# Kernel optimization log

Measured on AMD Instinct MI355X. Metric: run time of the kernel, lower is better.

Reference implementation:

```python
import jax, jax.numpy as jnp
import numpy as np

NUM_TAGS = 19
START_ID = 17  # lbl_to_id['START_LBL']
PAD_ID = 18    # lbl_to_id['PAD_LBL']
NEG = -1000.0


def setup_inputs() -> dict:
    key = jax.random.key(0)
    k1, k2, k3 = jax.random.split(key, 3)
    B, L = 512, 2048
    P = jax.random.normal(k1, (B, L, NUM_TAGS), dtype=jnp.float32)
    T = jax.random.normal(k2, (NUM_TAGS, NUM_TAGS), dtype=jnp.float32)
    # contiguous-prefix valid mask, lengths in [1, L]
    lengths = jax.random.randint(k3, (B,), 1, L + 1)
    mask = jnp.arange(L)[None, :] < lengths[:, None]  # [B, L] bool
    return {"P": P, "T": T, "mask": mask}


def _viterbi_forward(P, T, mask):
    # P: [B, L, K] emissions; T[j, k] = score of transition prev=k -> cur=j
    B, L, K = P.shape
    DP0 = jnp.full((B, K), NEG, dtype=P.dtype).at[:, START_ID].set(0.0)

    def step(DP, xs):
        emit, m = xs  # emit: [B, K], m: [B] bool
        scores = DP[:, None, :] + T[None, :, :]        # [B, cur, prev]
        best = scores.max(axis=-1)                      # [B, K]
        arg = scores.argmax(axis=-1).astype(jnp.int32)  # [B, K] backpointers
        new_DP = best + emit
        DP = jnp.where(m[:, None], new_DP, DP)          # frozen past sequence end
        return DP, arg

    DP, choice = jax.lax.scan(
        step, DP0, (jnp.swapaxes(P, 0, 1), jnp.swapaxes(mask, 0, 1))
    )  # choice: [L, B, K]
    DP = DP + T[PAD_ID][None, :]  # transition into PAD at the end
    return DP, choice


def reference(P, T, mask):
    B, L, K = P.shape
    DP, choice = _viterbi_forward(P, T, mask)
    last = DP.argmax(axis=-1).astype(jnp.int32)          # [B] best final tag
    lengths = mask.sum(axis=-1).astype(jnp.int32)        # [B]
    bidx = jnp.arange(B)

    def back(c, t):
        # path[t] = choice[t+1][path[t+1]] for t < len-1; path[len-1] = last
        nxt = choice[jnp.minimum(t + 1, L - 1), bidx, c]  # [B]
        new_c = jnp.where(t < lengths - 1, nxt, c)
        out = jnp.where(t < lengths, new_c, -1)           # -1 pads beyond length
        return new_c, out

    _, outs = jax.lax.scan(back, last, jnp.arange(L - 1, -1, -1))  # [L, B]
    path = jnp.flip(jnp.swapaxes(outs, 0, 1), axis=1)  # [B, L], decoded tags
    return path
```

## Files before the change

kernel.cpp:

```cpp
#include <hip/hip_runtime.h>

#define Bn 512
#define Ln 2048
#define Kn 19
#define NEGV (-1000.0f)
#define START_IDn 17
#define PAD_IDn 18
#define SEG 64
#define PBYTES 79691776u


#define DP_CORE(BASE)                                                          \
    float4 q0 = *(const float4*)((BASE) + 0);                                  \
    float4 q1 = *(const float4*)((BASE) + 4);                                  \
    float4 q2 = *(const float4*)((BASE) + 8);                                  \
    float4 q3 = *(const float4*)((BASE) + 12);                                 \
    float4 q4 = *(const float4*)((BASE) + 16);            \
    float cand[Kn];                                                            \
    cand[0]  = q0.x + Trow[0];  cand[1]  = q0.y + Trow[1];                     \
    cand[2]  = q0.z + Trow[2];  cand[3]  = q0.w + Trow[3];                     \
    cand[4]  = q1.x + Trow[4];  cand[5]  = q1.y + Trow[5];                     \
    cand[6]  = q1.z + Trow[6];  cand[7]  = q1.w + Trow[7];                     \
    cand[8]  = q2.x + Trow[8];  cand[9]  = q2.y + Trow[9];                     \
    cand[10] = q2.z + Trow[10]; cand[11] = q2.w + Trow[11];                    \
    cand[12] = q3.x + Trow[12]; cand[13] = q3.y + Trow[13];                    \
    cand[14] = q3.z + Trow[14]; cand[15] = q3.w + Trow[15];                    \
    cand[16] = q4.x + Trow[16]; cand[17] = q4.y + Trow[17];                    \
    cand[18] = q4.z + Trow[18];                                                \
    float m0 = fmaxf(fmaxf(cand[0],  cand[1]),  cand[2]);                      \
    float m1 = fmaxf(fmaxf(cand[3],  cand[4]),  cand[5]);                      \
    float m2 = fmaxf(fmaxf(cand[6],  cand[7]),  cand[8]);                      \
    float m3 = fmaxf(fmaxf(cand[9],  cand[10]), cand[11]);                     \
    float m4 = fmaxf(fmaxf(cand[12], cand[13]), cand[14]);                     \
    float m5 = fmaxf(fmaxf(cand[15], cand[16]), cand[17]);                     \
    float n0 = fmaxf(fmaxf(m0, m1), m2);                                       \
    float n1 = fmaxf(fmaxf(m3, m4), cand[18]);                                 \
    float best = fmaxf(fmaxf(n0, n1), m5);

__global__ __launch_bounds__(64, 1) void crf_fwd(
    const float* __restrict__ P, const float* __restrict__ T,
    const int* __restrict__ mask, float* __restrict__ dpck,
    float* __restrict__ dpfin, int* __restrict__ lens)
{
    const int lane = threadIdx.x;
    const int half = lane >> 5;
    const int c = lane & 31;
    const int b = blockIdx.x * 2 + half;
    const int cc = (c < Kn) ? c : (Kn - 1);

    float Trow[Kn];
#pragma unroll
    for (int p = 0; p < Kn; ++p) Trow[p] = T[cc * Kn + p];

    const int* mrow = mask + (size_t)b * Ln;
    int sum = 0;
#pragma unroll
    for (int j = 0; j < Ln / 128; ++j) {
        int4 v = *(const int4*)(mrow + j * 128 + c * 4);
        sum += v.x + v.y + v.z + v.w;
    }
#pragma unroll
    for (int k = 1; k < 32; k <<= 1) sum += __shfl_xor(sum, k, 64);
    const int len = sum;
    if (c == 0) lens[b] = len;
    const int lenO = __shfl_xor(len, 32, 64);
    int maxlen = len > lenO ? len : lenO;
    int lmin = len < lenO ? len : lenO;
    lmin = __builtin_amdgcn_readfirstlane(lmin);
    int mlen = (maxlen + (SEG - 1)) & ~(SEG - 1);
    mlen = __builtin_amdgcn_readfirstlane(mlen);

    __shared__ float dp[2][32];
    __shared__ float ebuf[2][2][1280];

    float mydp = (c == START_IDn) ? 0.0f : NEGV;
    dp[half][c] = mydp;

    const unsigned bbyte = (unsigned)b * (Ln * Kn * 4u);
    const unsigned limit = PBYTES - 16;
    const char* Pc = (const char*)P;
    float4 r[10];

#define STAGE_LOAD(ci)                                                         \
    { unsigned base_ = bbyte + (unsigned)(ci) * 4864u + ((unsigned)c << 4);    \
      _Pragma("unroll")                                                        \
      for (int i_ = 0; i_ < 10; ++i_) {                                        \
          unsigned o_ = base_ + (unsigned)i_ * 512u;                           \
          if (o_ > limit) o_ = limit;                                          \
          r[i_] = *(const float4*)(Pc + o_);                                   \
      } }
#define STAGE_WRITE(nb)                                                        \
    { float* d_ = &ebuf[nb][half][(unsigned)c << 2];                           \
      _Pragma("unroll")                                                        \
      for (int i_ = 0; i_ < 10; ++i_) *(float4*)(d_ + i_ * 128) = r[i_]; }

    int buf = 0;
    STAGE_LOAD(0);
    STAGE_WRITE(0);

    for (int t0 = 0; t0 < mlen; t0 += SEG) {
        if (c < Kn)
            dpck[((unsigned)b * 32u + (unsigned)(t0 >> 6)) * (unsigned)Kn + (unsigned)c] = mydp;
        STAGE_LOAD((t0 >> 6) + 1);
        const float* ebl = &ebuf[buf][half][0];

        if (t0 + SEG <= lmin) {
            for (int tt = 0; tt < SEG; tt += 8) {
#pragma unroll
                for (int u = 0; u < 8; ++u) {
                    const float e = ebl[(tt + u) * Kn + cc];
                    const float* base_ = &dp[half][0];
                    DP_CORE(base_)
                    mydp = best + e;
                    dp[half][c] = mydp;
                }
            }
        } else {
            for (int tt = 0; tt < SEG; tt += 8) {
#pragma unroll
                for (int u = 0; u < 8; ++u) {
                    const int t = t0 + tt + u;
                    const float e = ebl[(tt + u) * Kn + cc];
                    const float* base_ = &dp[half][0];
                    DP_CORE(base_)
                    float nd = best + e;
                    mydp = (t < len) ? nd : mydp;
                    dp[half][c] = mydp;
                }
            }
        }
        STAGE_WRITE(buf ^ 1);
        buf ^= 1;
    }
    if (c < Kn) dpfin[b * Kn + c] = mydp;
#undef STAGE_LOAD
#undef STAGE_WRITE
}

__global__ __launch_bounds__(256) void crf_rec(
    const float* __restrict__ P, const float* __restrict__ T,
    const float* __restrict__ dpck, const int* __restrict__ lens,
    unsigned char* __restrict__ choice)
{
    const int tid = threadIdx.x;
    const int halfid = tid >> 5;
    const int c = tid & 31;
    const int cc = (c < Kn) ? c : (Kn - 1);
    const int task = blockIdx.x * 8 + halfid;
    const int b = task >> 5;
    const int seg = task & 31;
    const int t0 = seg * SEG;
    const int len = lens[b];
    if (t0 >= len) return;

    __shared__ float dp[8][32];
    __shared__ __align__(16) unsigned char cbuf[8][SEG * Kn];

    float Trow[Kn];
#pragma unroll
    for (int p = 0; p < Kn; ++p) Trow[p] = T[cc * Kn + p];

    float mydp = (c < Kn) ? dpck[((unsigned)b * 32u + (unsigned)seg) * (unsigned)Kn + (unsigned)c]
                          : NEGV;
    dp[halfid][c] = mydp;

    const float* prow = P + (size_t)b * Ln * Kn + (size_t)t0 * Kn;

    float eb[8];
#pragma unroll
    for (int u = 0; u < 8; ++u) eb[u] = prow[u * Kn + cc];

    for (int tt = 0; tt < SEG; tt += 8) {
#pragma unroll
        for (int u = 0; u < 8; ++u) {
            const int t = t0 + tt + u;
            const float e = eb[u];
            const float* base_ = &dp[halfid][0];
            DP_CORE(base_)
            float nd = best + e;
            mydp = (t < len) ? nd : mydp;
            dp[halfid][c] = mydp;

            int arg = Kn - 1;
#pragma unroll
            for (int p = Kn - 2; p >= 0; --p)
                arg = (cand[p] == best) ? p : arg;
            if (c < Kn) cbuf[halfid][(tt + u) * Kn + c] = (unsigned char)arg;

            int tn = tt + u + 8;
            int tloc = (t0 + tn < Ln) ? tn : (Ln - 1 - t0);
            eb[u] = prow[tloc * Kn + cc];
        }
    }
    {
        const int4* s = (const int4*)&cbuf[halfid][0];
        int4* d = (int4*)(choice + (size_t)b * Ln * Kn + (size_t)t0 * Kn);
        for (int i = c; i < (SEG * Kn) / 16; i += 32) d[i] = s[i];
    }
}

__global__ __launch_bounds__(384, 1) void crf_bwd(
    const float* __restrict__ T, const unsigned char* __restrict__ choice,
    const float* __restrict__ dpfin, const int* __restrict__ lens,
    int* __restrict__ out)
{
    __shared__ unsigned char comp[Ln * Kn];
    __shared__ int vchain[17];
    __shared__ int s_last, s_len;

    const int b = blockIdx.x;
    const int tid = threadIdx.x;

    {
        const int4* src = (const int4*)(choice + (size_t)b * Ln * Kn);
        int4* dst = (int4*)comp;
        for (int i = tid; i < (Ln * Kn) / 16; i += 384) dst[i] = src[i];
    }
    if (tid == 0) {
        s_len = lens[b];
        float bestv = dpfin[b * Kn + 0] + T[PAD_IDn * Kn + 0];
        int bl = 0;
        for (int ci = 1; ci < Kn; ++ci) {
            float v = dpfin[b * Kn + ci] + T[PAD_IDn * Kn + ci];
            if (v > bestv) { bestv = v; bl = ci; }
        }
        s_last = bl;
    }
    __syncthreads();
    const int len = s_len;

    {
        const int wv = tid >> 6;
        const int lane = tid & 63;
        const int ch = wv * 3 + lane / Kn;
        const int c = lane % Kn;
        if (lane < 3 * Kn && ch < 16) {
            int cur = c;
            const int tb = ch * 128 + 127;
            for (int i = 0; i < 128; ++i) {
                const int t = tb - i;
                int nv = comp[t * Kn + cur];
                cur = (t < len) ? nv : cur;
                comp[t * Kn + c] = cur;
            }
        }
    }
    __syncthreads();

    if (tid == 0) {
        int v = s_last;
        vchain[16] = v;
        for (int ch = 15; ch >= 0; --ch) {
            v = comp[ch * 128 * Kn + v];
            vchain[ch] = v;
        }
    }
    __syncthreads();

    const int last = s_last;
    int* orow = out + (size_t)b * Ln;
    for (int t = tid; t < Ln; t += 384) {
        int val;
        if (t >= len) {
            val = -1;
        } else if (t == Ln - 1) {
            val = last;
        } else {
            const int tp = t + 1;
            const int vc = vchain[(tp >> 7) + 1];
            val = comp[tp * Kn + vc];
        }
        orow[t] = val;
    }
}

extern "C" void kernel_launch(void* const* d_in, const int* in_sizes, int n_in,
                              void* d_out, int out_size, void* d_ws, size_t ws_size,
                              hipStream_t stream)
{
    const float* P    = (const float*)d_in[0];
    const float* T    = (const float*)d_in[1];
    const int*   mask = (const int*)d_in[2];
    int* out = (int*)d_out;

    const size_t choice_bytes = (size_t)Bn * Ln * Kn;
    unsigned char* choice = (unsigned char*)d_ws;
    float* dpfin = (float*)((char*)d_ws + choice_bytes);
    int* lens = (int*)((char*)d_ws + choice_bytes + (size_t)Bn * Kn * 4);

    float* dpck = (float*)((char*)d_out + 2 * 1024 * 1024);

    crf_fwd<<<Bn / 2, 64, 0, stream>>>(P, T, mask, dpck, dpfin, lens);
    crf_rec<<<(Bn * 32) / 8, 256, 0, stream>>>(P, T, dpck, lens, choice);
    crf_bwd<<<Bn, 384, 0, stream>>>(T, choice, dpfin, lens, out);
}
```

Measured before the change: 398.2 us.

## Use one wave per sequence with readlane broadcast in forward Viterbi

The forward pass now gives each 64-lane wave a single sequence instead of packing two sequences per wave. The 19 previous DP values are broadcast with scalar readlane instead of an LDS store and reload each step. The loop runs only to the sequence's own length, with an exact remainder tail, so the masked select and the wasted steps caused by the longer partner sequence disappear. In exchange the launch uses twice as many blocks, and the 19 readlanes per step may serialise on the scalar path.

```diff
diff --git a/kernel.cpp b/kernel.cpp
--- a/kernel.cpp
+++ b/kernel.cpp
@@ -9,6 +9,118 @@
 #define SEG 64
 #define PBYTES 79691776u
 
+
+__global__ __launch_bounds__(64, 1) void crf_fwd(
+    const float* __restrict__ P, const float* __restrict__ T,
+    const int* __restrict__ mask, float* __restrict__ dpck,
+    float* __restrict__ dpfin, int* __restrict__ lens)
+{
+    const int lane = threadIdx.x;
+    const int b = blockIdx.x;
+    const int cc = (lane < Kn) ? lane : (Kn - 1);
+
+    float Trow[Kn];
+#pragma unroll
+    for (int p = 0; p < Kn; ++p) Trow[p] = T[cc * Kn + p];
+
+    const int* mrow = mask + (size_t)b * Ln;
+    int sum = 0;
+#pragma unroll
+    for (int j = 0; j < 8; ++j) {
+        int4 v = *(const int4*)(mrow + j * 256 + lane * 4);
+        sum += v.x + v.y + v.z + v.w;
+    }
+#pragma unroll
+    for (int k = 1; k < 64; k <<= 1) sum += __shfl_xor(sum, k, 64);
+    int lenr = __builtin_amdgcn_readfirstlane(sum);
+    if (lenr < 1) lenr = 1;
+    if (lenr > Ln) lenr = Ln;
+    const int len = lenr;
+    if (lane == 0) lens[b] = len;
+
+    __shared__ float ebuf[2][1232];
+
+    float mydp = (lane == START_IDn) ? 0.0f : NEGV;
+
+    const unsigned bbyte = (unsigned)b * (Ln * Kn * 4u);
+    const unsigned limit = PBYTES - 16;
+    const char* Pc = (const char*)P;
+    float4 r[5];
+
+#define STAGE_LOAD(ci)                                                         \
+    { unsigned sb_ = bbyte + (unsigned)(ci) * 4864u;                           \
+      _Pragma("unroll")                                                        \
+      for (int i_ = 0; i_ < 5; ++i_) {                                         \
+          unsigned idx_ = (unsigned)lane + 64u * (unsigned)i_;                 \
+          if (idx_ > 303u) idx_ = 303u;                                        \
+          unsigned o_ = sb_ + idx_ * 16u;                                      \
+          if (o_ > limit) o_ = limit;                                          \
+          r[i_] = *(const float4*)(Pc + o_);                                   \
+      } }
+#define STAGE_WRITE(nb)                                                        \
+    { _Pragma("unroll")                                                        \
+      for (int i_ = 0; i_ < 5; ++i_) {                                         \
+          unsigned idx_ = (unsigned)lane + 64u * (unsigned)i_;                 \
+          if (idx_ > 303u) idx_ = 303u;                                        \
+          *(float4*)((char*)&ebuf[nb][0] + idx_ * 16u) = r[i_];                \
+      } }
+
+#define RL(p) __int_as_float(__builtin_amdgcn_readlane(mi_, (p)))
+#define STEP_BODY(EXPR_E)                                                      \
+    { const float e_ = (EXPR_E);                                               \
+      const int mi_ = __float_as_int(mydp);                                    \
+      float c0_  = RL(0)  + Trow[0];  float c1_  = RL(1)  + Trow[1];           \
+      float c2_  = RL(2)  + Trow[2];  float c3_  = RL(3)  + Trow[3];           \
+      float c4_  = RL(4)  + Trow[4];  float c5_  = RL(5)  + Trow[5];           \
+      float c6_  = RL(6)  + Trow[6];  float c7_  = RL(7)  + Trow[7];           \
+      float c8_  = RL(8)  + Trow[8];  float c9_  = RL(9)  + Trow[9];           \
+      float c10_ = RL(10) + Trow[10]; float c11_ = RL(11) + Trow[11];          \
+      float c12_ = RL(12) + Trow[12]; float c13_ = RL(13) + Trow[13];          \
+      float c14_ = RL(14) + Trow[14]; float c15_ = RL(15) + Trow[15];          \
+      float c16_ = RL(16) + Trow[16]; float c17_ = RL(17) + Trow[17];          \
+      float c18_ = RL(18) + Trow[18];                                          \
+      float t0_ = fmaxf(fmaxf(c0_,  c1_),  c2_);                               \
+      float t1_ = fmaxf(fmaxf(c3_,  c4_),  c5_);                               \
+      float t2_ = fmaxf(fmaxf(c6_,  c7_),  c8_);                               \
+      float t3_ = fmaxf(fmaxf(c9_,  c10_), c11_);                              \
+      float t4_ = fmaxf(fmaxf(c12_, c13_), c14_);                              \
+      float t5_ = fmaxf(fmaxf(c15_, c16_), c17_);                              \
+      float u0_ = fmaxf(fmaxf(t0_, t1_), t2_);                                 \
+      float u1_ = fmaxf(fmaxf(t3_, t4_), c18_);                                \
+      float best_ = fmaxf(fmaxf(u0_, u1_), t5_);                               \
+      mydp = best_ + e_; }
+
+    int buf = 0;
+    STAGE_LOAD(0);
+    STAGE_WRITE(0);
+
+    const int nfull = len >> 6;
+    const int rem = len & 63;
+
+    for (int seg = 0; seg < nfull; ++seg) {
+        if (lane < Kn)
+            dpck[((unsigned)b * 32u + (unsigned)seg) * (unsigned)Kn + (unsigned)lane] = mydp;
+        STAGE_LOAD(seg + 1);
+        const float* ebl = &ebuf[buf][0];
+        for (int t8 = 0; t8 < SEG; t8 += 8) {
+#pragma unroll
+            for (int u = 0; u < 8; ++u) STEP_BODY(ebl[(t8 + u) * Kn + cc]);
+        }
+        STAGE_WRITE(buf ^ 1);
+        buf ^= 1;
+    }
+    if (rem) {
+        if (lane < Kn)
+            dpck[((unsigned)b * 32u + (unsigned)nfull) * (unsigned)Kn + (unsigned)lane] = mydp;
+        const float* ebl = &ebuf[buf][0];
+        for (int tt = 0; tt < rem; ++tt) STEP_BODY(ebl[tt * Kn + cc]);
+    }
+    if (lane < Kn) dpfin[b * Kn + lane] = mydp;
+#undef STAGE_LOAD
+#undef STAGE_WRITE
+#undef STEP_BODY
+#undef RL
+}
 
 #define DP_CORE(BASE)                                                          \
     float4 q0 = *(const float4*)((BASE) + 0);                                  \
@@ -37,106 +149,6 @@
     float n1 = fmaxf(fmaxf(m3, m4), cand[18]);                                 \
     float best = fmaxf(fmaxf(n0, n1), m5);
 
-__global__ __launch_bounds__(64, 1) void crf_fwd(
-    const float* __restrict__ P, const float* __restrict__ T,
-    const int* __restrict__ mask, float* __restrict__ dpck,
-    float* __restrict__ dpfin, int* __restrict__ lens)
-{
-    const int lane = threadIdx.x;
-    const int half = lane >> 5;
-    const int c = lane & 31;
-    const int b = blockIdx.x * 2 + half;
-    const int cc = (c < Kn) ? c : (Kn - 1);
-
-    float Trow[Kn];
-#pragma unroll
-    for (int p = 0; p < Kn; ++p) Trow[p] = T[cc * Kn + p];
-
-    const int* mrow = mask + (size_t)b * Ln;
-    int sum = 0;
-#pragma unroll
-    for (int j = 0; j < Ln / 128; ++j) {
-        int4 v = *(const int4*)(mrow + j * 128 + c * 4);
-        sum += v.x + v.y + v.z + v.w;
-    }
-#pragma unroll
-    for (int k = 1; k < 32; k <<= 1) sum += __shfl_xor(sum, k, 64);
-    const int len = sum;
-    if (c == 0) lens[b] = len;
-    const int lenO = __shfl_xor(len, 32, 64);
-    int maxlen = len > lenO ? len : lenO;
-    int lmin = len < lenO ? len : lenO;
-    lmin = __builtin_amdgcn_readfirstlane(lmin);
-    int mlen = (maxlen + (SEG - 1)) & ~(SEG - 1);
-    mlen = __builtin_amdgcn_readfirstlane(mlen);
-
-    __shared__ float dp[2][32];
-    __shared__ float ebuf[2][2][1280];
-
-    float mydp = (c == START_IDn) ? 0.0f : NEGV;
-    dp[half][c] = mydp;
-
-    const unsigned bbyte = (unsigned)b * (Ln * Kn * 4u);
-    const unsigned limit = PBYTES - 16;
-    const char* Pc = (const char*)P;
-    float4 r[10];
-
-#define STAGE_LOAD(ci)                                                         \
-    { unsigned base_ = bbyte + (unsigned)(ci) * 4864u + ((unsigned)c << 4);    \
-      _Pragma("unroll")                                                        \
-      for (int i_ = 0; i_ < 10; ++i_) {                                        \
-          unsigned o_ = base_ + (unsigned)i_ * 512u;                           \
-          if (o_ > limit) o_ = limit;                                          \
-          r[i_] = *(const float4*)(Pc + o_);                                   \
-      } }
-#define STAGE_WRITE(nb)                                                        \
-    { float* d_ = &ebuf[nb][half][(unsigned)c << 2];                           \
-      _Pragma("unroll")                                                        \
-      for (int i_ = 0; i_ < 10; ++i_) *(float4*)(d_ + i_ * 128) = r[i_]; }
-
-    int buf = 0;
-    STAGE_LOAD(0);
-    STAGE_WRITE(0);
-
-    for (int t0 = 0; t0 < mlen; t0 += SEG) {
-        if (c < Kn)
-            dpck[((unsigned)b * 32u + (unsigned)(t0 >> 6)) * (unsigned)Kn + (unsigned)c] = mydp;
-        STAGE_LOAD((t0 >> 6) + 1);
-        const float* ebl = &ebuf[buf][half][0];
-
-        if (t0 + SEG <= lmin) {
-            for (int tt = 0; tt < SEG; tt += 8) {
-#pragma unroll
-                for (int u = 0; u < 8; ++u) {
-                    const float e = ebl[(tt + u) * Kn + cc];
-                    const float* base_ = &dp[half][0];
-                    DP_CORE(base_)
-                    mydp = best + e;
-                    dp[half][c] = mydp;
-                }
-            }
-        } else {
-            for (int tt = 0; tt < SEG; tt += 8) {
-#pragma unroll
-                for (int u = 0; u < 8; ++u) {
-                    const int t = t0 + tt + u;
-                    const float e = ebl[(tt + u) * Kn + cc];
-                    const float* base_ = &dp[half][0];
-                    DP_CORE(base_)
-                    float nd = best + e;
-                    mydp = (t < len) ? nd : mydp;
-                    dp[half][c] = mydp;
-                }
-            }
-        }
-        STAGE_WRITE(buf ^ 1);
-        buf ^= 1;
-    }
-    if (c < Kn) dpfin[b * Kn + c] = mydp;
-#undef STAGE_LOAD
-#undef STAGE_WRITE
-}
-
 __global__ __launch_bounds__(256) void crf_rec(
     const float* __restrict__ P, const float* __restrict__ T,
     const float* __restrict__ dpck, const int* __restrict__ lens,
@@ -290,7 +302,7 @@
 
     float* dpck = (float*)((char*)d_out + 2 * 1024 * 1024);
 
-    crf_fwd<<<Bn / 2, 64, 0, stream>>>(P, T, mask, dpck, dpfin, lens);
+    crf_fwd<<<Bn, 64, 0, stream>>>(P, T, mask, dpck, dpfin, lens);
     crf_rec<<<(Bn * 32) / 8, 256, 0, stream>>>(P, T, dpck, lens, choice);
     crf_bwd<<<Bn, 384, 0, stream>>>(T, choice, dpfin, lens, out);
 }
```

Measured after the change: 475.1 us. +19.3%, slower.

## Stage segment emissions in LDS with bulk float4 loads and trim loop to valid length

Applied to the files above, without the earlier changes.

The recompute kernel now loads each segment's whole emission block (64 steps x 19 tags) into shared memory up front with coalesced float4 loads, replacing the rolling 8-deep register prefetch of scalar global loads. The per-step loop reads emissions from LDS and runs only up to the valid remaining length, which drops the per-step length mask and the work done past the end of each sequence. It adds about 39 KB of LDS per block, which may reduce occupancy, and it places a load barrier at the start of each segment.

```diff
diff --git a/kernel.cpp b/kernel.cpp
--- a/kernel.cpp
+++ b/kernel.cpp
@@ -153,44 +153,56 @@
     const int len = lens[b];
     if (t0 >= len) return;
 
+    int rem = len - t0;
+    if (rem > SEG) rem = SEG;
+
     __shared__ float dp[8][32];
     __shared__ __align__(16) unsigned char cbuf[8][SEG * Kn];
+    __shared__ float ebuf[8][1232];
 
     float Trow[Kn];
 #pragma unroll
     for (int p = 0; p < Kn; ++p) Trow[p] = T[cc * Kn + p];
+
+    {
+        const unsigned sb = ((unsigned)b * (Ln * Kn * 4u)) + (unsigned)t0 * (Kn * 4u);
+        const unsigned limit = PBYTES - 16;
+        const char* Pc = (const char*)P;
+        float4 rr[10];
+#pragma unroll
+        for (int i = 0; i < 10; ++i) {
+            unsigned idx = (unsigned)c + 32u * (unsigned)i;
+            if (idx > 303u) idx = 303u;
+            unsigned o = sb + idx * 16u;
+            if (o > limit) o = limit;
+            rr[i] = *(const float4*)(Pc + o);
+        }
+        char* eb = (char*)&ebuf[halfid][0];
+#pragma unroll
+        for (int i = 0; i < 10; ++i) {
+            unsigned idx = (unsigned)c + 32u * (unsigned)i;
+            if (idx > 303u) idx = 303u;
+            *(float4*)(eb + idx * 16u) = rr[i];
+        }
+    }
 
     float mydp = (c < Kn) ? dpck[((unsigned)b * 32u + (unsigned)seg) * (unsigned)Kn + (unsigned)c]
                           : NEGV;
     dp[halfid][c] = mydp;
 
-    const float* prow = P + (size_t)b * Ln * Kn + (size_t)t0 * Kn;
-
-    float eb[8];
-#pragma unroll
-    for (int u = 0; u < 8; ++u) eb[u] = prow[u * Kn + cc];
-
-    for (int tt = 0; tt < SEG; tt += 8) {
-#pragma unroll
-        for (int u = 0; u < 8; ++u) {
-            const int t = t0 + tt + u;
-            const float e = eb[u];
-            const float* base_ = &dp[halfid][0];
-            DP_CORE(base_)
-            float nd = best + e;
-            mydp = (t < len) ? nd : mydp;
-            dp[halfid][c] = mydp;
-
-            int arg = Kn - 1;
-#pragma unroll
-            for (int p = Kn - 2; p >= 0; --p)
-                arg = (cand[p] == best) ? p : arg;
-            if (c < Kn) cbuf[halfid][(tt + u) * Kn + c] = (unsigned char)arg;
-
-            int tn = tt + u + 8;
-            int tloc = (t0 + tn < Ln) ? tn : (Ln - 1 - t0);
-            eb[u] = prow[tloc * Kn + cc];
-        }
+    const float* ebl = &ebuf[halfid][0];
+    for (int tt = 0; tt < rem; ++tt) {
+        const float e = ebl[tt * Kn + cc];
+        const float* base_ = &dp[halfid][0];
+        DP_CORE(base_)
+        mydp = best + e;
+        dp[halfid][c] = mydp;
+
+        int arg = Kn - 1;
+#pragma unroll
+        for (int p = Kn - 2; p >= 0; --p)
+            arg = (cand[p] == best) ? p : arg;
+        if (c < Kn) cbuf[halfid][tt * Kn + c] = (unsigned char)arg;
     }
     {
         const int4* s = (const int4*)&cbuf[halfid][0];
```

After: 415.5 us. 1.04x slower.

## Fuse segment recompute and backtrace into one kernel keeping backpointers in LDS

Applied to the files above, without the earlier changes.

Merges the per-segment backpointer recomputation kernel with the backtrace kernel. Each block now handles one batch row, and 16 half-waves each recompute two 64-step segments, writing argmax choices straight into a shared-memory buffer instead of global memory. This removes the global write and re-read of the roughly 20 MB choice array and one kernel launch. The cost is lower parallelism: 512 blocks with a two-pass loop, one block per CU because of about 39 KB of LDS, and a serial recompute depth doubled per half-wave. The dpck scratch also moves from the output buffer into the workspace.

```diff
diff --git a/kernel.cpp b/kernel.cpp
--- a/kernel.cpp
+++ b/kernel.cpp
@@ -137,112 +137,90 @@
 #undef STAGE_WRITE
 }
 
-__global__ __launch_bounds__(256) void crf_rec(
+__global__ __launch_bounds__(512, 1) void crf_recbt(
     const float* __restrict__ P, const float* __restrict__ T,
-    const float* __restrict__ dpck, const int* __restrict__ lens,
-    unsigned char* __restrict__ choice)
+    const float* __restrict__ dpck, const float* __restrict__ dpfin,
+    const int* __restrict__ lens, int* __restrict__ out)
 {
     const int tid = threadIdx.x;
-    const int halfid = tid >> 5;
+    const int b = blockIdx.x;
+    const int hw = tid >> 5;
     const int c = tid & 31;
     const int cc = (c < Kn) ? c : (Kn - 1);
-    const int task = blockIdx.x * 8 + halfid;
-    const int b = task >> 5;
-    const int seg = task & 31;
-    const int t0 = seg * SEG;
     const int len = lens[b];
-    if (t0 >= len) return;
-
-    __shared__ float dp[8][32];
-    __shared__ __align__(16) unsigned char cbuf[8][SEG * Kn];
+
+    __shared__ unsigned char comp[Ln * Kn];
+    __shared__ float dp[16][32];
+    __shared__ int vchain[17];
+    __shared__ int s_last;
 
     float Trow[Kn];
 #pragma unroll
     for (int p = 0; p < Kn; ++p) Trow[p] = T[cc * Kn + p];
 
-    float mydp = (c < Kn) ? dpck[((unsigned)b * 32u + (unsigned)seg) * (unsigned)Kn + (unsigned)c]
-                          : NEGV;
-    dp[halfid][c] = mydp;
-
-    const float* prow = P + (size_t)b * Ln * Kn + (size_t)t0 * Kn;
-
-    float eb[8];
-#pragma unroll
-    for (int u = 0; u < 8; ++u) eb[u] = prow[u * Kn + cc];
-
-    for (int tt = 0; tt < SEG; tt += 8) {
-#pragma unroll
-        for (int u = 0; u < 8; ++u) {
-            const int t = t0 + tt + u;
-            const float e = eb[u];
-            const float* base_ = &dp[halfid][0];
-            DP_CORE(base_)
-            float nd = best + e;
-            mydp = (t < len) ? nd : mydp;
-            dp[halfid][c] = mydp;
-
-            int arg = Kn - 1;
-#pragma unroll
-            for (int p = Kn - 2; p >= 0; --p)
-                arg = (cand[p] == best) ? p : arg;
-            if (c < Kn) cbuf[halfid][(tt + u) * Kn + c] = (unsigned char)arg;
-
-            int tn = tt + u + 8;
-            int tloc = (t0 + tn < Ln) ? tn : (Ln - 1 - t0);
-            eb[u] = prow[tloc * Kn + cc];
-        }
-    }
-    {
-        const int4* s = (const int4*)&cbuf[halfid][0];
-        int4* d = (int4*)(choice + (size_t)b * Ln * Kn + (size_t)t0 * Kn);
-        for (int i = c; i < (SEG * Kn) / 16; i += 32) d[i] = s[i];
-    }
-}
-
-__global__ __launch_bounds__(384, 1) void crf_bwd(
-    const float* __restrict__ T, const unsigned char* __restrict__ choice,
-    const float* __restrict__ dpfin, const int* __restrict__ lens,
-    int* __restrict__ out)
-{
-    __shared__ unsigned char comp[Ln * Kn];
-    __shared__ int vchain[17];
-    __shared__ int s_last, s_len;
-
-    const int b = blockIdx.x;
-    const int tid = threadIdx.x;
-
-    {
-        const int4* src = (const int4*)(choice + (size_t)b * Ln * Kn);
-        int4* dst = (int4*)comp;
-        for (int i = tid; i < (Ln * Kn) / 16; i += 384) dst[i] = src[i];
-    }
-    if (tid == 0) {
-        s_len = lens[b];
-        float bestv = dpfin[b * Kn + 0] + T[PAD_IDn * Kn + 0];
-        int bl = 0;
-        for (int ci = 1; ci < Kn; ++ci) {
-            float v = dpfin[b * Kn + ci] + T[PAD_IDn * Kn + ci];
-            if (v > bestv) { bestv = v; bl = ci; }
-        }
-        s_last = bl;
+#pragma unroll 1
+    for (int pass = 0; pass < 2; ++pass) {
+        const int seg = hw + pass * 16;
+        const int t0 = seg * SEG;
+        if (t0 < len) {
+            float mydp = (c < Kn)
+                ? dpck[((unsigned)b * 32u + (unsigned)seg) * (unsigned)Kn + (unsigned)c]
+                : NEGV;
+            dp[hw][c] = mydp;
+            const float* prow = P + (size_t)b * Ln * Kn + (size_t)t0 * Kn;
+
+            float eb[8];
+#pragma unroll
+            for (int u = 0; u < 8; ++u) eb[u] = prow[u * Kn + cc];
+
+            for (int tt = 0; tt < SEG; tt += 8) {
+#pragma unroll
+                for (int u = 0; u < 8; ++u) {
+                    const int t = t0 + tt + u;
+                    const float e = eb[u];
+                    const float* base_ = &dp[hw][0];
+                    DP_CORE(base_)
+                    float nd = best + e;
+                    mydp = (t < len) ? nd : mydp;
+                    dp[hw][c] = mydp;
+
+                    int arg = Kn - 1;
+#pragma unroll
+                    for (int p = Kn - 2; p >= 0; --p)
+                        arg = (cand[p] == best) ? p : arg;
+                    if (c < Kn) comp[t * Kn + c] = (unsigned char)arg;
+
+                    int tn = tt + u + 8;
+                    int tloc = (t0 + tn < Ln) ? tn : (Ln - 1 - t0);
+                    eb[u] = prow[tloc * Kn + cc];
+                }
+            }
+        }
     }
     __syncthreads();
-    const int len = s_len;
 
     {
         const int wv = tid >> 6;
         const int lane = tid & 63;
-        const int ch = wv * 3 + lane / Kn;
-        const int c = lane % Kn;
-        if (lane < 3 * Kn && ch < 16) {
-            int cur = c;
+        if (lane < 2 * Kn) {
+            const int ch = wv * 2 + lane / Kn;
+            const int c2 = lane % Kn;
+            int cur = c2;
             const int tb = ch * 128 + 127;
             for (int i = 0; i < 128; ++i) {
                 const int t = tb - i;
                 int nv = comp[t * Kn + cur];
                 cur = (t < len) ? nv : cur;
-                comp[t * Kn + c] = cur;
-            }
+                comp[t * Kn + c2] = cur;
+            }
+        } else if (tid == 511) {
+            float bestv = dpfin[b * Kn + 0] + T[PAD_IDn * Kn + 0];
+            int bl = 0;
+            for (int ci = 1; ci < Kn; ++ci) {
+                float v = dpfin[b * Kn + ci] + T[PAD_IDn * Kn + ci];
+                if (v > bestv) { bestv = v; bl = ci; }
+            }
+            s_last = bl;
         }
     }
     __syncthreads();
@@ -259,7 +237,7 @@
 
     const int last = s_last;
     int* orow = out + (size_t)b * Ln;
-    for (int t = tid; t < Ln; t += 384) {
+    for (int t = tid; t < Ln; t += 512) {
         int val;
         if (t >= len) {
             val = -1;
@@ -283,14 +261,11 @@
     const int*   mask = (const int*)d_in[2];
     int* out = (int*)d_out;
 
-    const size_t choice_bytes = (size_t)Bn * Ln * Kn;
-    unsigned char* choice = (unsigned char*)d_ws;
-    float* dpfin = (float*)((char*)d_ws + choice_bytes);
-    int* lens = (int*)((char*)d_ws + choice_bytes + (size_t)Bn * Kn * 4);
-
-    float* dpck = (float*)((char*)d_out + 2 * 1024 * 1024);
+    float* dpck  = (float*)d_ws;
+    float* dpfin = (float*)((char*)d_ws + (size_t)Bn * 32 * Kn * 4);
+    int*   lens  = (int*)((char*)d_ws + (size_t)Bn * 32 * Kn * 4
+                          + (size_t)Bn * Kn * 4);
 
     crf_fwd<<<Bn / 2, 64, 0, stream>>>(P, T, mask, dpck, dpfin, lens);
-    crf_rec<<<(Bn * 32) / 8, 256, 0, stream>>>(P, T, dpck, lens, choice);
-    crf_bwd<<<Bn, 384, 0, stream>>>(T, choice, dpfin, lens, out);
+    crf_recbt<<<Bn, 512, 0, stream>>>(P, T, dpck, dpfin, lens, out);
 }
```

After: 398.8 us. Within noise of the previous version (+0.2%).
